# Optimization experiments

Measured on AMD Instinct MI355X. Metric: run time of the kernel, lower is better.

## Reference

```python
import jax, jax.numpy as jnp
import numpy as np
import math

EMBED_DIM = 1024
NUM_HEADS = 16
HEAD_DIM = EMBED_DIM // NUM_HEADS
B, S = 2, 2048


def setup_inputs() -> dict:
    key = jax.random.key(0)
    ks = jax.random.split(key, 13)
    sc = 1.0 / math.sqrt(EMBED_DIM)
    inp = {
        "query": jax.random.normal(ks[0], (B, S, EMBED_DIM), jnp.float32),
        "key": jax.random.normal(ks[1], (B, S, EMBED_DIM), jnp.float32),
        "value": jax.random.normal(ks[2], (B, S, EMBED_DIM), jnp.float32),
        "input_patch_mask": jax.random.randint(ks[3], (B, S), 0, 2, jnp.int32),
        "Wq": jax.random.normal(ks[4], (EMBED_DIM, EMBED_DIM), jnp.float32) * sc,
        "bq": jnp.zeros((EMBED_DIM,), jnp.float32),
        "Wk": jax.random.normal(ks[5], (EMBED_DIM, EMBED_DIM), jnp.float32) * sc,
        "bk": jnp.zeros((EMBED_DIM,), jnp.float32),
        "Wv": jax.random.normal(ks[6], (EMBED_DIM, EMBED_DIM), jnp.float32) * sc,
        "bv": jnp.zeros((EMBED_DIM,), jnp.float32),
        "Wo": jax.random.normal(ks[7], (EMBED_DIM, EMBED_DIM), jnp.float32) * sc,
        "bo": jnp.zeros((EMBED_DIM,), jnp.float32),
    }
    return inp


def _masked_softmax(scores, mask):
    # Equivalent to masked_fill(-inf) -> softmax -> nan_to_num(0.0):
    # fully-masked rows produce exactly 0, without generating NaNs.
    neg_inf = jnp.array(-jnp.inf, scores.dtype)
    s = jnp.where(mask, scores, neg_inf)
    m = jnp.max(s, axis=-1, keepdims=True)
    m_safe = jnp.where(jnp.isfinite(m), m, jnp.zeros_like(m))
    e = jnp.where(mask, jnp.exp(s - m_safe), 0.0)
    denom = jnp.sum(e, axis=-1, keepdims=True)
    denom = jnp.where(denom == 0.0, 1.0, denom)
    return e / denom


def reference(query, key, value, input_patch_mask, Wq, bq, Wk, bk, Wv, bv, Wo, bo):
    b, s, d = query.shape
    h, hd = NUM_HEADS, HEAD_DIM
    q = (query @ Wq.T + bq).reshape(b, s, h, hd).transpose(0, 2, 1, 3)  # [b,h,s,hd]
    k = (key @ Wk.T + bk).reshape(b, s, h, hd).transpose(0, 2, 1, 3)
    v = (value @ Wv.T + bv).reshape(b, s, h, hd).transpose(0, 2, 1, 3)
    scores = jnp.einsum("bhqd,bhkd->bhqk", q, k) / math.sqrt(hd)
    # mask[b,i,j] = patch_mask[b,i] * patch_mask[b,j]
    mask = (input_patch_mask[:, :, None] * input_patch_mask[:, None, :]) > 0
    attn = _masked_softmax(scores, mask[:, None, :, :])  # dropout in eval mode = identity
    context = jnp.einsum("bhqk,bhkd->bhqd", attn, v)
    context = context.transpose(0, 2, 1, 3).reshape(b, s, d)
    return context @ Wo.T + bo
```

## Files before the change

### kernel.cpp

```cpp
#include <hip/hip_runtime.h>
#include <cstdint>
#include <cstddef>

#define EMBED 1024
#define NHEAD 16
#define HD    64
#define BATCH 2
#define SEQ   2048
#define MROWS (BATCH*SEQ)
#define QSCALE 0.1803368801111137f

typedef __bf16 bf16;
typedef __bf16 bf16x8 __attribute__((ext_vector_type(8)));
typedef float  f32x4  __attribute__((ext_vector_type(4)));
typedef unsigned int u32;

#if __has_builtin(__builtin_amdgcn_exp2f)
#define EXP2(x) __builtin_amdgcn_exp2f(x)
#else
#define EXP2(x) exp2f(x)
#endif

typedef const u32 __attribute__((address_space(1)))* gp_t;
typedef u32 __attribute__((address_space(3)))* lp_t;

__device__ __forceinline__ void g2l16(const void* g, void* l) {
  __builtin_amdgcn_global_load_lds((gp_t)(uintptr_t)g, (lp_t)(u32)(uintptr_t)l, 16, 0, 0);
}

__device__ __forceinline__ void pipeline_barrier() {
  asm volatile("s_waitcnt vmcnt(0)" ::: "memory");
  __builtin_amdgcn_s_barrier();
  __builtin_amdgcn_sched_barrier(0);
}

#define MFMA(a, b, c) __builtin_amdgcn_mfma_f32_16x16x32_bf16((a), (b), (c), 0, 0, 0)

#define SZX8 ((MROWS*EMBED)/8)
#define SZW8 ((EMBED*EMBED)/8)

__global__ void cast_all(const float* __restrict__ q, const float* __restrict__ k,
                         const float* __restrict__ v, const float* __restrict__ wq,
                         const float* __restrict__ wk, const float* __restrict__ wv,
                         const float* __restrict__ wo,
                         bf16* xq, bf16* xk, bf16* xv,
                         bf16* wqb, bf16* wkb, bf16* wvb, bf16* wob) {
  int z = blockIdx.y;
  const float* in; bf16* out;
  switch (z) {
    case 0: in = q;  out = xq;  break;
    case 1: in = k;  out = xk;  break;
    case 2: in = v;  out = xv;  break;
    case 3: in = wq; out = wqb; break;
    case 4: in = wk; out = wkb; break;
    case 5: in = wv; out = wvb; break;
    default: in = wo; out = wob; break;
  }
  int n8 = (z < 3) ? SZX8 : SZW8;
  int i = blockIdx.x * blockDim.x + threadIdx.x;
  if (i >= n8) return;
  const float4* p = (const float4*)in;
  float4 a = p[2*i], b = p[2*i+1];
  union { bf16 h[8]; uint4 u; } r;
  r.h[0] = (bf16)a.x; r.h[1] = (bf16)a.y; r.h[2] = (bf16)a.z; r.h[3] = (bf16)a.w;
  r.h[4] = (bf16)b.x; r.h[5] = (bf16)b.y; r.h[6] = (bf16)b.z; r.h[7] = (bf16)b.w;
  ((uint4*)out)[i] = r.u;
}

#define BM 128
#define BN 128
#define BK 32
#define NKI (EMBED/BK)

__device__ __forceinline__ void gemm_core(
    const bf16* __restrict__ A, const bf16* __restrict__ W,
    int m0, int n0, bf16* Al, bf16* Bl, f32x4 (&acc)[4][4])
{
  const int tid  = threadIdx.x;
  const int lane = tid & 63, wid = tid >> 6;
  const int quad = lane >> 4, l16 = lane & 15;
  const int wm = wid >> 1, wn = wid & 1;

  const int R = tid >> 2, Cc = tid & 3;
  const int gcol = (Cc ^ ((R >> 1) & 3)) * 8;
  const bf16* Ag = A + (size_t)(m0 + R) * EMBED + gcol;
  const bf16* Bg = W + (size_t)(n0 + R) * EMBED + gcol;
  bf16* AlW = Al + wid * 512;
  bf16* BlW = Bl + wid * 512;

  g2l16(Ag, AlW);                      g2l16(Ag + (size_t)64*EMBED, AlW + 2048);
  g2l16(Bg, BlW);                      g2l16(Bg + (size_t)64*EMBED, BlW + 2048);

  for (int ki = 0; ki < NKI; ++ki) {
    pipeline_barrier();
    if (ki + 1 < NKI) {
      const int nb = (ki + 1) & 1;
      const int k0 = (ki + 1) * BK;
      g2l16(Ag + k0, AlW + nb*4096);
      g2l16(Ag + (size_t)64*EMBED + k0, AlW + nb*4096 + 2048);
      g2l16(Bg + k0, BlW + nb*4096);
      g2l16(Bg + (size_t)64*EMBED + k0, BlW + nb*4096 + 2048);
    }
    const bf16* Ac = Al + (ki & 1)*4096;
    const bf16* Bc = Bl + (ki & 1)*4096;
    bf16x8 af[4], bg[4];
#pragma unroll
    for (int i = 0; i < 4; ++i) {
      int ra = wm*64 + i*16 + l16;
      af[i] = *(const bf16x8*)(Ac + ra*32 + ((quad ^ ((ra>>1)&3))*8));
      int rb = wn*64 + i*16 + l16;
      bg[i] = *(const bf16x8*)(Bc + rb*32 + ((quad ^ ((rb>>1)&3))*8));
    }
#pragma unroll
    for (int i = 0; i < 4; ++i)
#pragma unroll
      for (int j = 0; j < 4; ++j)
        acc[i][j] = MFMA(af[i], bg[j], acc[i][j]);
  }
}

__global__ __launch_bounds__(256) void qkv_kernel(
    const bf16* __restrict__ Xq, const bf16* __restrict__ Xk, const bf16* __restrict__ Xv,
    const bf16* __restrict__ Wq, const bf16* __restrict__ Wk, const bf16* __restrict__ Wv,
    const float* __restrict__ bq, const float* __restrict__ bk, const float* __restrict__ bv,
    bf16* __restrict__ Qp, bf16* __restrict__ Kp, bf16* __restrict__ VTg)
{
  __shared__ bf16 Al[2*BM*BK];
  __shared__ bf16 Bl[2*BN*BK];
  const int z = blockIdx.z;
  const bf16* A = z==0 ? Xq : z==1 ? Xk : Wv;
  const bf16* W = z==0 ? Wq : z==1 ? Wk : Xv;
  const float* bias = z==0 ? bq : z==1 ? bk : bv;
  const float scale = (z==0) ? QSCALE : 1.0f;
  const int m0 = (z < 2) ? blockIdx.y * BM : blockIdx.x * BM;
  const int n0 = (z < 2) ? blockIdx.x * BN : blockIdx.y * BN;

  f32x4 acc[4][4] = {};
  gemm_core(A, W, m0, n0, Al, Bl, acc);

  const int lane = threadIdx.x & 63, wid = threadIdx.x >> 6;
  const int quad = lane >> 4, l16 = lane & 15;
  const int wm = wid >> 1, wn = wid & 1;

  if (z < 2) {
#pragma unroll
    for (int i = 0; i < 4; ++i) {
#pragma unroll
      for (int j = 0; j < 4; ++j) {
        int col = n0 + wn*64 + j*16 + l16;
        float bv2 = bias[col];
        bf16* outp = (z == 0) ? Qp : Kp;
#pragma unroll
        for (int r = 0; r < 4; ++r) {
          int row = m0 + wm*64 + i*16 + quad*4 + r;
          outp[(size_t)row*EMBED + col] = (bf16)((acc[i][j][r] + bv2) * scale);
        }
      }
    }
  } else {
    const int tcol0 = n0 + wn*64;
    const int bb   = tcol0 >> 11;
    const int tile = (tcol0 & (SEQ-1)) >> 6;
    const int pbase = (l16 >> 2)*8 + (l16 & 3)*2;
#pragma unroll
    for (int i = 0; i < 4; ++i) {
      float4 bv4 = *(const float4*)&bias[m0 + wm*64 + i*16 + quad*4];
#pragma unroll
      for (int r = 0; r < 4; ++r) {
        int e = m0 + wm*64 + i*16 + quad*4 + r;
        int hh = e >> 6, dd = e & (HD-1);
        float bvr = (r==0) ? bv4.x : (r==1) ? bv4.y : (r==2) ? bv4.z : bv4.w;
        union { bf16 h[2]; u32 u; } p01, p23;
        p01.h[0] = (bf16)(acc[i][0][r] + bvr);
        p01.h[1] = (bf16)(acc[i][1][r] + bvr);
        p23.h[0] = (bf16)(acc[i][2][r] + bvr);
        p23.h[1] = (bf16)(acc[i][3][r] + bvr);
        size_t base = (((size_t)bb*NHEAD + hh)*HD + dd)*SEQ + tile*64;
        *(u32*)&VTg[base + pbase]      = p01.u;
        *(u32*)&VTg[base + 32 + pbase] = p23.u;
      }
    }
  }
}

__global__ __launch_bounds__(256) void oproj_kernel(
    const bf16* __restrict__ Ctx, const bf16* __restrict__ Wo,
    const float* __restrict__ bo, float* __restrict__ out)
{
  __shared__ bf16 Al[2*128*32];
  __shared__ bf16 Bl[2*64*32];
  const int tid  = threadIdx.x;
  const int lane = tid & 63, wid = tid >> 6;
  const int quad = lane >> 4, l16 = lane & 15;
  const int m0 = blockIdx.y * 128, n0 = blockIdx.x * 64;

  const int R = tid >> 2, Cc = tid & 3;
  const int gcol = (Cc ^ ((R >> 1) & 3)) * 8;
  const bf16* Ag = Ctx + (size_t)(m0 + R) * EMBED + gcol;
  const bf16* Bg = Wo  + (size_t)(n0 + R) * EMBED + gcol;
  bf16* AlW = Al + wid * 512;
  bf16* BlW = Bl + wid * 512;

  g2l16(Ag, AlW);  g2l16(Ag + (size_t)64*EMBED, AlW + 2048);
  g2l16(Bg, BlW);

  f32x4 acc[2][4] = {};
  for (int ki = 0; ki < NKI; ++ki) {
    pipeline_barrier();
    if (ki + 1 < NKI) {
      const int nb = (ki + 1) & 1;
      const int k0 = (ki + 1) * BK;
      g2l16(Ag + k0, AlW + nb*4096);
      g2l16(Ag + (size_t)64*EMBED + k0, AlW + nb*4096 + 2048);
      g2l16(Bg + k0, BlW + nb*2048);
    }
    const bf16* Ac = Al + (ki & 1)*4096;
    const bf16* Bc = Bl + (ki & 1)*2048;
    bf16x8 af[2], bg[4];
#pragma unroll
    for (int u = 0; u < 2; ++u) {
      int ra = wid*32 + u*16 + l16;
      af[u] = *(const bf16x8*)(Ac + ra*32 + ((quad ^ ((ra>>1)&3))*8));
    }
#pragma unroll
    for (int j = 0; j < 4; ++j) {
      int rb = j*16 + l16;
      bg[j] = *(const bf16x8*)(Bc + rb*32 + ((quad ^ ((rb>>1)&3))*8));
    }
#pragma unroll
    for (int u = 0; u < 2; ++u)
#pragma unroll
      for (int j = 0; j < 4; ++j)
        acc[u][j] = MFMA(af[u], bg[j], acc[u][j]);
  }

#pragma unroll
  for (int u = 0; u < 2; ++u)
#pragma unroll
    for (int j = 0; j < 4; ++j) {
      int col = n0 + j*16 + l16;
      float bv = bo[col];
#pragma unroll
      for (int r = 0; r < 4; ++r) {
        int row = m0 + wid*32 + u*16 + quad*4 + r;
        out[(size_t)row*EMBED + col] = (acc[u][j][r] + bv);
      }
    }
}

#define NT  (SEQ/64)

__global__ __launch_bounds__(512, 2) void attn_kernel(
    const bf16* __restrict__ Qp, const bf16* __restrict__ Kp, const bf16* __restrict__ VT,
    const int* __restrict__ pmask, bf16* __restrict__ Ctx)
{
  __shared__ __align__(16) bf16 SM[5*4096];

  const int qt = blockIdx.x, h = blockIdx.y, b = blockIdx.z;
  const int tid = threadIdx.x, lane = tid & 63, wid = tid >> 6;
  const int quad = lane >> 4, l16 = lane & 15;
  const int w4 = wid & 3, h2 = wid >> 2;
  const int qrow0 = qt*128 + w4*32;

  bf16x8 qf[2][2];
#pragma unroll
  for (int qg = 0; qg < 2; ++qg) {
    const size_t qoff = (size_t)(b*SEQ + qrow0 + qg*16 + l16)*EMBED + h*HD;
    qf[qg][0] = *(const bf16x8*)(Qp + qoff + quad*8);
    qf[qg][1] = *(const bf16x8*)(Qp + qoff + 32 + quad*8);
  }

  bf16 onev = (bf16)1.0f;
  bf16x8 ones = {onev, onev, onev, onev, onev, onev, onev, onev};

  const bf16* Kg  = Kp + (size_t)b*SEQ*EMBED + h*HD;
  const bf16* VTg = VT + (size_t)(b*NHEAD + h)*HD*SEQ;
  const int*  kmw = pmask + b*SEQ + h2*32 + quad*4;

  const int R = tid >> 3;
  const int Cc = tid & 7;
  const int scol = (Cc ^ (R & 7)) * 8;

  f32x4 o[2][4] = {};
  f32x4 lacc[2] = {};
  bf16x8 pa[2] = {};

#define STAGE_K(kt, buf) g2l16(Kg + (size_t)((kt)*64 + R)*EMBED + scol, SM + (buf)*4096 + wid*512)
#define STAGE_V(kt, buf) g2l16(VTg + (size_t)R*SEQ + (kt)*64 + scol,    SM + 8192 + (buf)*4096 + wid*512)

  int4 kq0 = *(const int4*)(kmw);
  int4 kq1 = *(const int4*)(kmw + 16);
  STAGE_K(0, 0);
  STAGE_V(0, 0);

  for (int kt = 0; kt < NT; ++kt) {
    asm volatile("s_waitcnt vmcnt(0)" ::: "memory");
    __builtin_amdgcn_s_barrier();
    __builtin_amdgcn_sched_barrier(0);

    float fm0[4], fm1[4];
    fm0[0] = (float)kq0.x; fm0[1] = (float)kq0.y; fm0[2] = (float)kq0.z; fm0[3] = (float)kq0.w;
    fm1[0] = (float)kq1.x; fm1[1] = (float)kq1.y; fm1[2] = (float)kq1.z; fm1[3] = (float)kq1.w;
    __builtin_amdgcn_sched_barrier(0);

    if (kt + 1 < NT) {
      kq0 = *(const int4*)(kmw + (kt+1)*64);
      kq1 = *(const int4*)(kmw + (kt+1)*64 + 16);
      STAGE_K(kt + 1, (kt + 1) & 1);
      STAGE_V(kt + 1, (kt + 1) % 3);
    }

    if (kt > 0) {
      const bf16* Vc = SM + 8192 + ((kt - 1) % 3)*4096;
      lacc[0] = MFMA(pa[0], ones, lacc[0]);
      lacc[1] = MFMA(pa[1], ones, lacc[1]);
#pragma unroll
      for (int t = 0; t < 4; ++t) {
        int rd = t*16 + l16, sd = rd & 7;
        bf16x8 vf = *(const bf16x8*)(Vc + rd*64 + (((h2*4 + quad) ^ sd)*8));
        o[0][t] = MFMA(pa[0], vf, o[0][t]);
        o[1][t] = MFMA(pa[1], vf, o[1][t]);
      }
    }

    const bf16* Kc = SM + (kt & 1)*4096;
#pragma unroll
    for (int kg = 0; kg < 2; ++kg) {
      int ra = h2*32 + kg*16 + l16, sa = ra & 7;
      bf16x8 kfa = *(const bf16x8*)(Kc + ra*64 + ((quad       ^ sa)*8));
      bf16x8 kfb = *(const bf16x8*)(Kc + ra*64 + (((quad + 4) ^ sa)*8));
      const float* fm = kg ? fm1 : fm0;
#pragma unroll
      for (int qg = 0; qg < 2; ++qg) {
        f32x4 s = {};
        s = MFMA(kfa, qf[qg][0], s);
        s = MFMA(kfb, qf[qg][1], s);
        pa[qg][0 + kg] = (bf16)(EXP2(s[0]) * fm[0]);
        pa[qg][2 + kg] = (bf16)(EXP2(s[1]) * fm[1]);
        pa[qg][4 + kg] = (bf16)(EXP2(s[2]) * fm[2]);
        pa[qg][6 + kg] = (bf16)(EXP2(s[3]) * fm[3]);
      }
    }
  }

  {
    const bf16* Vc = SM + 8192 + ((NT - 1) % 3)*4096;
    lacc[0] = MFMA(pa[0], ones, lacc[0]);
    lacc[1] = MFMA(pa[1], ones, lacc[1]);
#pragma unroll
    for (int t = 0; t < 4; ++t) {
      int rd = t*16 + l16, sd = rd & 7;
      bf16x8 vf = *(const bf16x8*)(Vc + rd*64 + (((h2*4 + quad) ^ sd)*8));
      o[0][t] = MFMA(pa[0], vf, o[0][t]);
      o[1][t] = MFMA(pa[1], vf, o[1][t]);
    }
  }

  __syncthreads();
  f32x4* rp = (f32x4*)SM;
  const int idx = w4*64 + lane;
  if (h2 == 1) {
#pragma unroll
    for (int qg = 0; qg < 2; ++qg) {
#pragma unroll
      for (int t = 0; t < 4; ++t) rp[(qg*4 + t)*256 + idx] = o[qg][t];
      rp[2048 + qg*256 + idx] = lacc[qg];
    }
  }
  __syncthreads();
  if (h2 == 0) {
#pragma unroll
    for (int qg = 0; qg < 2; ++qg) {
      lacc[qg] += rp[2048 + qg*256 + idx];
#pragma unroll
      for (int t = 0; t < 4; ++t) o[qg][t] += rp[(qg*4 + t)*256 + idx];
    }
#pragma unroll
    for (int qg = 0; qg < 2; ++qg) {
      int4 qm = *(const int4*)(pmask + b*SEQ + qrow0 + qg*16 + quad*4);
      float inv[4];
      inv[0] = (qm.x && lacc[qg][0] > 0.f) ? 1.0f / lacc[qg][0] : 0.0f;
      inv[1] = (qm.y && lacc[qg][1] > 0.f) ? 1.0f / lacc[qg][1] : 0.0f;
      inv[2] = (qm.z && lacc[qg][2] > 0.f) ? 1.0f / lacc[qg][2] : 0.0f;
      inv[3] = (qm.w && lacc[qg][3] > 0.f) ? 1.0f / lacc[qg][3] : 0.0f;
#pragma unroll
      for (int t = 0; t < 4; ++t)
#pragma unroll
        for (int r = 0; r < 4; ++r) {
          int row = b*SEQ + qrow0 + qg*16 + quad*4 + r;
          Ctx[(size_t)row*EMBED + h*HD + t*16 + l16] = (bf16)(o[qg][t][r] * inv[r]);
        }
    }
  }
}

extern "C" void kernel_launch(void* const* d_in, const int* in_sizes, int n_in,
                              void* d_out, int out_size, void* d_ws, size_t ws_size,
                              hipStream_t stream)
{
  const float* query = (const float*)d_in[0];
  const float* key   = (const float*)d_in[1];
  const float* value = (const float*)d_in[2];
  const int*   pm    = (const int*)d_in[3];
  const float* Wq = (const float*)d_in[4];
  const float* bq = (const float*)d_in[5];
  const float* Wk = (const float*)d_in[6];
  const float* bk = (const float*)d_in[7];
  const float* Wv = (const float*)d_in[8];
  const float* bv = (const float*)d_in[9];
  const float* Wo = (const float*)d_in[10];
  const float* bo = (const float*)d_in[11];
  float* out = (float*)d_out;

  const size_t SZ_X = (size_t)MROWS * EMBED;
  const size_t SZ_W = (size_t)EMBED * EMBED;

  bf16* p   = (bf16*)d_ws;
  bf16* Xq  = p; p += SZ_X;
  bf16* Xk  = p; p += SZ_X;
  bf16* Xv  = p; p += SZ_X;
  bf16* Wqb = p; p += SZ_W;
  bf16* Wkb = p; p += SZ_W;
  bf16* Wvb = p; p += SZ_W;
  bf16* Wob = p; p += SZ_W;
  bf16* Qp  = p; p += SZ_X;
  bf16* Kp  = p; p += SZ_X;
  bf16* VTg = p; p += SZ_X;
  bf16* Ctx = p; p += SZ_X;

  dim3 gc((unsigned)(SZX8/256), 7);
  cast_all<<<gc, 256, 0, stream>>>(query, key, value, Wq, Wk, Wv, Wo,
                                   Xq, Xk, Xv, Wqb, Wkb, Wvb, Wob);

  dim3 gq(EMBED/BN, MROWS/BM, 3);
  qkv_kernel<<<gq, 256, 0, stream>>>(Xq, Xk, Xv, Wqb, Wkb, Wvb, bq, bk, bv, Qp, Kp, VTg);

  dim3 ga(SEQ/128, NHEAD, BATCH);
  attn_kernel<<<ga, 512, 0, stream>>>(Qp, Kp, VTg, pm, Ctx);

  dim3 gg(EMBED/64, MROWS/128);
  oproj_kernel<<<gg, 256, 0, stream>>>(Ctx, Wob, bo, out);
}
```

Before: 231.5 us.

## Triple-buffer GEMM global-to-LDS loads and remap block order for locality

Changes the QKV and output-projection GEMMs from double to triple buffering in LDS. Two stages are kept in flight, and a partial vmcnt wait replaces the full drain each iteration, so global load latency can overlap more compute. It also remaps block indices so that consecutive hardware blocks are spread across tiles, aiming at better L2 reuse. LDS use grows by half, which may reduce occupancy, and the attention kernel is untouched.

```diff
diff --git a/kernel.cpp b/kernel.cpp
--- a/kernel.cpp
+++ b/kernel.cpp
@@ -26,12 +26,6 @@
 
 __device__ __forceinline__ void g2l16(const void* g, void* l) {
   __builtin_amdgcn_global_load_lds((gp_t)(uintptr_t)g, (lp_t)(u32)(uintptr_t)l, 16, 0, 0);
-}
-
-__device__ __forceinline__ void pipeline_barrier() {
-  asm volatile("s_waitcnt vmcnt(0)" ::: "memory");
-  __builtin_amdgcn_s_barrier();
-  __builtin_amdgcn_sched_barrier(0);
 }
 
 #define MFMA(a, b, c) __builtin_amdgcn_mfma_f32_16x16x32_bf16((a), (b), (c), 0, 0, 0)
@@ -88,21 +82,25 @@
   bf16* AlW = Al + wid * 512;
   bf16* BlW = Bl + wid * 512;
 
-  g2l16(Ag, AlW);                      g2l16(Ag + (size_t)64*EMBED, AlW + 2048);
-  g2l16(Bg, BlW);                      g2l16(Bg + (size_t)64*EMBED, BlW + 2048);
+#define GSTAGE(ki) do { \
+    const int nb_ = (ki) % 3; const int k0_ = (ki) * BK; \
+    g2l16(Ag + k0_,                    AlW + nb_*4096); \
+    g2l16(Ag + (size_t)64*EMBED + k0_, AlW + nb_*4096 + 2048); \
+    g2l16(Bg + k0_,                    BlW + nb_*4096); \
+    g2l16(Bg + (size_t)64*EMBED + k0_, BlW + nb_*4096 + 2048); } while (0)
+
+  GSTAGE(0);
+  GSTAGE(1);
 
   for (int ki = 0; ki < NKI; ++ki) {
-    pipeline_barrier();
-    if (ki + 1 < NKI) {
-      const int nb = (ki + 1) & 1;
-      const int k0 = (ki + 1) * BK;
-      g2l16(Ag + k0, AlW + nb*4096);
-      g2l16(Ag + (size_t)64*EMBED + k0, AlW + nb*4096 + 2048);
-      g2l16(Bg + k0, BlW + nb*4096);
-      g2l16(Bg + (size_t)64*EMBED + k0, BlW + nb*4096 + 2048);
-    }
-    const bf16* Ac = Al + (ki & 1)*4096;
-    const bf16* Bc = Bl + (ki & 1)*4096;
+    if (ki < NKI - 1) asm volatile("s_waitcnt vmcnt(4)" ::: "memory");
+    else              asm volatile("s_waitcnt vmcnt(0)" ::: "memory");
+    __builtin_amdgcn_s_barrier();
+    __builtin_amdgcn_sched_barrier(0);
+    if (ki + 2 < NKI) GSTAGE(ki + 2);
+
+    const bf16* Ac = Al + (ki % 3)*4096;
+    const bf16* Bc = Bl + (ki % 3)*4096;
     bf16x8 af[4], bg[4];
 #pragma unroll
     for (int i = 0; i < 4; ++i) {
@@ -117,6 +115,7 @@
       for (int j = 0; j < 4; ++j)
         acc[i][j] = MFMA(af[i], bg[j], acc[i][j]);
   }
+#undef GSTAGE
 }
 
 __global__ __launch_bounds__(256) void qkv_kernel(
@@ -125,15 +124,21 @@
     const float* __restrict__ bq, const float* __restrict__ bk, const float* __restrict__ bv,
     bf16* __restrict__ Qp, bf16* __restrict__ Kp, bf16* __restrict__ VTg)
 {
-  __shared__ bf16 Al[2*BM*BK];
-  __shared__ bf16 Bl[2*BN*BK];
-  const int z = blockIdx.z;
+  __shared__ bf16 Al[3*BM*BK];
+  __shared__ bf16 Bl[3*BN*BK];
+
+  const unsigned hw = blockIdx.x + 8u*blockIdx.y + 256u*blockIdx.z;
+  const unsigned wk = (hw & 7u)*96u + (hw >> 3);
+  const int z  = (int)(wk >> 8);
+  const unsigned rem = wk & 255u;
+  const int by = (int)(rem >> 3), bx = (int)(rem & 7u);
+
   const bf16* A = z==0 ? Xq : z==1 ? Xk : Wv;
   const bf16* W = z==0 ? Wq : z==1 ? Wk : Xv;
   const float* bias = z==0 ? bq : z==1 ? bk : bv;
   const float scale = (z==0) ? QSCALE : 1.0f;
-  const int m0 = (z < 2) ? blockIdx.y * BM : blockIdx.x * BM;
-  const int n0 = (z < 2) ? blockIdx.x * BN : blockIdx.y * BN;
+  const int m0 = (z < 2) ? by * BM : bx * BM;
+  const int n0 = (z < 2) ? bx * BN : by * BN;
 
   f32x4 acc[4][4] = {};
   gemm_core(A, W, m0, n0, Al, Bl, acc);
@@ -187,12 +192,15 @@
     const bf16* __restrict__ Ctx, const bf16* __restrict__ Wo,
     const float* __restrict__ bo, float* __restrict__ out)
 {
-  __shared__ bf16 Al[2*128*32];
-  __shared__ bf16 Bl[2*64*32];
+  __shared__ bf16 Al[3*128*32];
+  __shared__ bf16 Bl[3*64*32];
   const int tid  = threadIdx.x;
   const int lane = tid & 63, wid = tid >> 6;
   const int quad = lane >> 4, l16 = lane & 15;
-  const int m0 = blockIdx.y * 128, n0 = blockIdx.x * 64;
+
+  const unsigned hw = blockIdx.x + 16u*blockIdx.y;
+  const unsigned wk = (hw & 7u)*64u + (hw >> 3);
+  const int m0 = (int)(wk >> 4) * 128, n0 = (int)(wk & 15u) * 64;
 
   const int R = tid >> 2, Cc = tid & 3;
   const int gcol = (Cc ^ ((R >> 1) & 3)) * 8;
@@ -201,21 +209,25 @@
   bf16* AlW = Al + wid * 512;
   bf16* BlW = Bl + wid * 512;
 
-  g2l16(Ag, AlW);  g2l16(Ag + (size_t)64*EMBED, AlW + 2048);
-  g2l16(Bg, BlW);
+#define OSTAGE(ki) do { \
+    const int nb_ = (ki) % 3; const int k0_ = (ki) * BK; \
+    g2l16(Ag + k0_,                    AlW + nb_*4096); \
+    g2l16(Ag + (size_t)64*EMBED + k0_, AlW + nb_*4096 + 2048); \
+    g2l16(Bg + k0_,                    BlW + nb_*2048); } while (0)
+
+  OSTAGE(0);
+  OSTAGE(1);
 
   f32x4 acc[2][4] = {};
   for (int ki = 0; ki < NKI; ++ki) {
-    pipeline_barrier();
-    if (ki + 1 < NKI) {
-      const int nb = (ki + 1) & 1;
-      const int k0 = (ki + 1) * BK;
-      g2l16(Ag + k0, AlW + nb*4096);
-      g2l16(Ag + (size_t)64*EMBED + k0, AlW + nb*4096 + 2048);
-      g2l16(Bg + k0, BlW + nb*2048);
-    }
-    const bf16* Ac = Al + (ki & 1)*4096;
-    const bf16* Bc = Bl + (ki & 1)*2048;
+    if (ki < NKI - 1) asm volatile("s_waitcnt vmcnt(3)" ::: "memory");
+    else              asm volatile("s_waitcnt vmcnt(0)" ::: "memory");
+    __builtin_amdgcn_s_barrier();
+    __builtin_amdgcn_sched_barrier(0);
+    if (ki + 2 < NKI) OSTAGE(ki + 2);
+
+    const bf16* Ac = Al + (ki % 3)*4096;
+    const bf16* Bc = Bl + (ki % 3)*2048;
     bf16x8 af[2], bg[4];
 #pragma unroll
     for (int u = 0; u < 2; ++u) {
@@ -233,6 +245,7 @@
       for (int j = 0; j < 4; ++j)
         acc[u][j] = MFMA(af[u], bg[j], acc[u][j]);
   }
+#undef OSTAGE
 
 #pragma unroll
   for (int u = 0; u < 2; ++u)
```

Result: faster. 216.3 us (-6.6%).
